# Kernel optimization log

Measured on AMD Instinct MI355X. Metric: run time of the kernel, lower is better.

Reference implementation:

```python
import jax, jax.numpy as jnp
import numpy as np

N_NODES = 50000
N_EDGES = 1_600_000
DIMS = [512, 256, 128]


def _edge_softmax(vals, rows, n):
    # sparse softmax over dim=1 (per source row), only over stored edges
    m = jax.ops.segment_max(vals, rows, num_segments=n)
    e = jnp.exp(vals - m[rows])
    s = jax.ops.segment_sum(e, rows, num_segments=n)
    return e / s[rows]


def _spmm(att, rows, cols, H, n):
    # (sparse C) @ H : gather source cols, scale by edge weight, scatter-add to rows
    return jax.ops.segment_sum(att[:, None] * H[cols], rows, num_segments=n)


def setup_inputs() -> dict:
    key = jax.random.key(0)
    ks = jax.random.split(key, 12)
    X = jax.random.normal(ks[0], (N_NODES, DIMS[0]), dtype=jnp.float32)
    edge_row = jax.random.randint(ks[1], (N_EDGES,), 0, N_NODES, dtype=jnp.int32)
    edge_col = jax.random.randint(ks[2], (N_EDGES,), 0, N_NODES, dtype=jnp.int32)
    A_vals = jnp.ones((N_EDGES,), dtype=jnp.float32)
    def lin(k, dout, din):
        lim = 1.0 / np.sqrt(din)
        return jax.random.uniform(k, (dout, din), jnp.float32, -lim, lim)
    W0 = lin(ks[3], DIMS[1], DIMS[0])
    b0 = jax.random.uniform(ks[4], (DIMS[1],), jnp.float32, -1/np.sqrt(DIMS[0]), 1/np.sqrt(DIMS[0]))
    W1 = lin(ks[5], DIMS[2], DIMS[1])
    b1 = jax.random.uniform(ks[6], (DIMS[2],), jnp.float32, -1/np.sqrt(DIMS[1]), 1/np.sqrt(DIMS[1]))
    v00 = jax.random.normal(ks[7], (DIMS[1],), dtype=jnp.float32)
    v01 = jax.random.normal(ks[8], (DIMS[1],), dtype=jnp.float32)
    v10 = jax.random.normal(ks[9], (DIMS[2],), dtype=jnp.float32)
    v11 = jax.random.normal(ks[10], (DIMS[2],), dtype=jnp.float32)
    return {"X": X, "edge_row": edge_row, "edge_col": edge_col, "A_vals": A_vals,
            "W0": W0, "b0": b0, "W1": W1, "b1": b1,
            "v00": v00, "v01": v01, "v10": v10, "v11": v11}


def reference(X, edge_row, edge_col, A_vals, W0, b0, W1, b1, v00, v01, v10, v11):
    n = X.shape[0]
    layers = [((W0, b0), (v00, v01)), ((W1, b1), (v10, v11))]
    H = X
    atts = []
    # encoder
    for (W, b), (va, vb) in layers:
        M = H @ W.T + b                               # [N, d_out]
        # attention logits are computed under no_grad in the original
        f1 = M @ va                                   # [N]
        f2 = M @ vb
        logits = jax.lax.stop_gradient(A_vals * (f1[edge_row] + f2[edge_col]))
        att = _edge_softmax(jax.nn.sigmoid(logits), edge_row, n)
        H = _spmm(att, edge_row, edge_col, M, n)
        atts.append(att)
    final_H = H
    # decoder (tied weights, reverse order, reuse encoder attention)
    for ((W, _), _), att in zip(reversed(layers), reversed(atts)):
        H = H @ W                                     # F.linear(H, W.t()) == H @ W
        H = _spmm(att, edge_row, edge_col, H, n)
    return H, final_H
```

## Files before the change

### kernel.cpp

```cpp
#include <hip/hip_runtime.h>
#include <cstdint>
#include <cstddef>

typedef __attribute__((ext_vector_type(8))) short bf16x8;
typedef __attribute__((ext_vector_type(4))) float f32x4;

__device__ __forceinline__ ushort f2b(float f) {
    union { float f; uint32_t u; } v; v.f = f;
    uint32_t r = (v.u + 0x7fffu + ((v.u >> 16) & 1u)) >> 16;
    return (ushort)r;
}
__device__ __forceinline__ float b2f(ushort b) {
    union { uint32_t u; float f; } v; v.u = ((uint32_t)b) << 16;
    return v.f;
}

__device__ __forceinline__ void gll16(const void* g, void* l) {
    __builtin_amdgcn_global_load_lds((const __attribute__((address_space(1))) void*)g,
                                     (__attribute__((address_space(3))) void*)l, 16, 0, 0);
}

__global__ __launch_bounds__(256) void hist_kernel(const int* __restrict__ rows,
                                                   int* __restrict__ bhist, int E, int nb) {
    __shared__ int h[512];
    for (int i = threadIdx.x; i < nb; i += 256) h[i] = 0;
    __syncthreads();
    int stride = gridDim.x * blockDim.x;
    for (int e = blockIdx.x * blockDim.x + threadIdx.x; e < E; e += stride)
        atomicAdd(&h[rows[e] >> 7], 1);
    __syncthreads();
    for (int i = threadIdx.x; i < nb; i += 256)
        if (h[i]) atomicAdd(&bhist[i], h[i]);
}

__global__ __launch_bounds__(512) void scan512(const int* __restrict__ bhist,
                                               int* __restrict__ boff, int* __restrict__ gcur,
                                               int* __restrict__ rp, int nb, int E, int N) {
    __shared__ int sm[512];
    int v = ((int)threadIdx.x < nb) ? bhist[threadIdx.x] : 0;
    sm[threadIdx.x] = v;
    __syncthreads();
    for (int off = 1; off < 512; off <<= 1) {
        int t = ((int)threadIdx.x >= off) ? sm[threadIdx.x - off] : 0;
        __syncthreads();
        sm[threadIdx.x] += t;
        __syncthreads();
    }
    if ((int)threadIdx.x < nb) {
        int e0 = sm[threadIdx.x] - v;
        boff[threadIdx.x] = e0;
        gcur[threadIdx.x] = e0;
    }
    if (threadIdx.x == 0) { boff[nb] = E; rp[N] = E; }
}

__global__ __launch_bounds__(256) void binpass(const int* __restrict__ rows,
                                               const int* __restrict__ cols,
                                               const float* __restrict__ avals,
                                               int* __restrict__ gcur,
                                               uint2* __restrict__ tmp, int E, int nb) {
    __shared__ int hist[512];
    __shared__ int base[512];
    int e0 = blockIdx.x * 4096;
    int nE = min(4096, E - e0);
    for (int i = threadIdx.x; i < nb; i += 256) hist[i] = 0;
    __syncthreads();
    for (int i = threadIdx.x; i < nE; i += 256)
        atomicAdd(&hist[rows[e0 + i] >> 7], 1);
    __syncthreads();
    for (int i = threadIdx.x; i < nb; i += 256) {
        int c = hist[i];
        if (c) base[i] = atomicAdd(&gcur[i], c);
        hist[i] = 0;
    }
    __syncthreads();
    for (int i = threadIdx.x; i < nE; i += 256) {
        int r = rows[e0 + i];
        int b = r >> 7;
        int loc = atomicAdd(&hist[b], 1);
        uint2 t;
        t.x = ((uint32_t)r << 16) | (uint32_t)cols[e0 + i];
        t.y = __float_as_uint(avals[e0 + i]);
        tmp[base[b] + loc] = t;
    }
}

__global__ __launch_bounds__(256) void bucketpass(const uint2* __restrict__ tmp,
                                                  const int* __restrict__ boff,
                                                  int* __restrict__ rp,
                                                  int* __restrict__ col_s,
                                                  float* __restrict__ a_s, int N) {
    __shared__ int cnt[128];
    __shared__ int pre[128];
    int b = blockIdx.x;
    int r0 = b << 7;
    int nr = min(128, N - r0);
    int t0 = boff[b], t1 = boff[b + 1];
    if ((int)threadIdx.x < 128) cnt[threadIdx.x] = 0;
    __syncthreads();
    for (int i = t0 + (int)threadIdx.x; i < t1; i += 256)
        atomicAdd(&cnt[(tmp[i].x >> 16) - r0], 1);
    __syncthreads();
    if ((int)threadIdx.x < 128) pre[threadIdx.x] = cnt[threadIdx.x];
    __syncthreads();
    for (int off = 1; off < 128; off <<= 1) {
        int t = ((int)threadIdx.x >= off && (int)threadIdx.x < 128) ? pre[threadIdx.x - off] : 0;
        __syncthreads();
        if ((int)threadIdx.x < 128) pre[threadIdx.x] += t;
        __syncthreads();
    }
    if ((int)threadIdx.x < nr) {
        int ex = pre[threadIdx.x] - cnt[threadIdx.x];
        rp[r0 + threadIdx.x] = t0 + ex;
        cnt[threadIdx.x] = t0 + ex;
    }
    __syncthreads();
    for (int i = t0 + (int)threadIdx.x; i < t1; i += 256) {
        uint2 t = tmp[i];
        int lr = (int)(t.x >> 16) - r0;
        int pos = atomicAdd(&cnt[lr], 1);
        col_s[pos] = (int)(t.x & 0xffffu);
        a_s[pos] = __uint_as_float(t.y);
    }
}

__global__ void f2b4_kernel(const float* __restrict__ src, ushort* __restrict__ dst, int n4) {
    int i = blockIdx.x * blockDim.x + threadIdx.x;
    if (i < n4) {
        float4 v = ((const float4*)src)[i];
        ushort4 o;
        o.x = f2b(v.x); o.y = f2b(v.y); o.z = f2b(v.z); o.w = f2b(v.w);
        ((ushort4*)dst)[i] = o;
    }
}

__global__ __launch_bounds__(256) void prep_weights(const float* __restrict__ W0,
                                                    const float* __restrict__ W1,
                                                    ushort* __restrict__ W0h,
                                                    ushort* __restrict__ W1h,
                                                    ushort* __restrict__ Wt0h) {
    int i = blockIdx.x * 256 + threadIdx.x;
    float4 v = ((const float4*)W0)[i];
    ushort4 o;
    o.x = f2b(v.x); o.y = f2b(v.y); o.z = f2b(v.z); o.w = f2b(v.w);
    ((ushort4*)W0h)[i] = o;
    int r = (i * 4) >> 9;
    int c = (i * 4) & 511;
    Wt0h[(size_t)(c + 0) * 256 + r] = o.x;
    Wt0h[(size_t)(c + 1) * 256 + r] = o.y;
    Wt0h[(size_t)(c + 2) * 256 + r] = o.z;
    Wt0h[(size_t)(c + 3) * 256 + r] = o.w;
    if (i < 8192) {
        float4 w = ((const float4*)W1)[i];
        ushort4 p;
        p.x = f2b(w.x); p.y = f2b(w.y); p.z = f2b(w.z); p.w = f2b(w.w);
        ((ushort4*)W1h)[i] = p;
    }
}

__global__ __launch_bounds__(256) void gemm_bf16(const ushort* __restrict__ A,
                                                 const ushort* __restrict__ B,
                                                 const float* __restrict__ bias,
                                                 float* __restrict__ Cf,
                                                 ushort* __restrict__ Ch,
                                                 int M, int K, int Dout) {
    __shared__ ushort As[128 * 64];
    __shared__ ushort Bs[128 * 64];
    int bm = blockIdx.y * 128, bn = blockIdx.x * 128;
    int tid = threadIdx.x;
    int w = tid >> 6, l = tid & 63;
    int wm = (w & 1) * 64, wn = (w >> 1) * 64;
    int lm = l & 15, quad = l >> 4;
    int wslot = tid & 192;

    f32x4 acc[4][4] = {};

    for (int k0 = 0; k0 < K; k0 += 64) {
#pragma unroll
        for (int it = 0; it < 4; ++it) {
            int slot = it * 256 + tid;
            int row = slot >> 3;
            int qg = ((slot & 7) ^ (row & 7)) * 8;
            int ga = bm + row; if (ga > M - 1) ga = M - 1;
            gll16(A + (size_t)ga * K + k0 + qg, As + (size_t)(it * 256 + wslot) * 8);
            gll16(B + (size_t)(bn + row) * K + k0 + qg, Bs + (size_t)(it * 256 + wslot) * 8);
        }
        __syncthreads();
#pragma unroll
        for (int ks = 0; ks < 2; ++ks) {
            bf16x8 af[4], bfr[4];
#pragma unroll
            for (int i = 0; i < 4; ++i) {
                int r = wm + i * 16 + lm;
                af[i] = *(const bf16x8*)&As[r * 64 + (((ks * 4 + quad) ^ (r & 7)) * 8)];
            }
#pragma unroll
            for (int j = 0; j < 4; ++j) {
                int r = wn + j * 16 + lm;
                bfr[j] = *(const bf16x8*)&Bs[r * 64 + (((ks * 4 + quad) ^ (r & 7)) * 8)];
            }
#pragma unroll
            for (int i = 0; i < 4; ++i)
#pragma unroll
                for (int j = 0; j < 4; ++j)
                    acc[i][j] = __builtin_amdgcn_mfma_f32_16x16x32_bf16(af[i], bfr[j], acc[i][j], 0, 0, 0);
        }
        __syncthreads();
    }

    float bv[4] = {0.f, 0.f, 0.f, 0.f};
    if (bias) {
#pragma unroll
        for (int j = 0; j < 4; ++j) bv[j] = bias[bn + wn + j * 16 + lm];
    }
#pragma unroll
    for (int i = 0; i < 4; ++i) {
#pragma unroll
        for (int r = 0; r < 4; ++r) {
            int row = bm + wm + i * 16 + quad * 4 + r;
            if (row < M) {
#pragma unroll
                for (int j = 0; j < 4; ++j) {
                    int col = bn + wn + j * 16 + lm;
                    float v = acc[i][j][r] + bv[j];
                    if (Cf) Cf[(size_t)row * Dout + col] = v;
                    if (Ch) Ch[(size_t)row * Dout + col] = f2b(v);
                }
            }
        }
    }
}

__global__ __launch_bounds__(256) void fvec256_kernel(const ushort* __restrict__ Mh,
                                                      const float* __restrict__ va,
                                                      const float* __restrict__ vb,
                                                      float* __restrict__ f1,
                                                      float* __restrict__ f2, int N) {
    int n = blockIdx.x * 4 + (threadIdx.x >> 6);
    if (n >= N) return;
    int lane = threadIdx.x & 63;
    ushort4 m4 = ((const ushort4*)(Mh + (size_t)n * 256))[lane];
    float4 a4 = ((const float4*)va)[lane];
    float4 b4 = ((const float4*)vb)[lane];
    float m0 = b2f(m4.x), m1 = b2f(m4.y), m2 = b2f(m4.z), m3 = b2f(m4.w);
    float s1 = m0 * a4.x + m1 * a4.y + m2 * a4.z + m3 * a4.w;
    float s2 = m0 * b4.x + m1 * b4.y + m2 * b4.z + m3 * b4.w;
#pragma unroll
    for (int off = 32; off > 0; off >>= 1) {
        s1 += __shfl_xor(s1, off);
        s2 += __shfl_xor(s2, off);
    }
    if (lane == 0) { f1[n] = s1; f2[n] = s2; }
}

__global__ __launch_bounds__(256) void att2_kernel(const int* __restrict__ rp,
                                                   const int* __restrict__ col_s,
                                                   const float* __restrict__ a_s,
                                                   const float* __restrict__ f1,
                                                   const float* __restrict__ f2,
                                                   float* __restrict__ att,
                                                   float* __restrict__ rs, int N) {
    int r = blockIdx.x * 4 + (threadIdx.x >> 6);
    if (r >= N) return;
    int lane = threadIdx.x & 63;
    int beg = rp[r], end = rp[r + 1];
    float fr = f1[r];
    float s = 0.f;
    for (int j = beg + lane; j < end; j += 64) {
        float x = a_s[j] * (fr + f2[col_s[j]]);
        float v = 1.f / (1.f + __expf(-x));
        float e = __expf(v);
        att[j] = e;
        s += e;
    }
#pragma unroll
    for (int off = 32; off > 0; off >>= 1) s += __shfl_xor(s, off);
    if (lane == 0) rs[r] = (end > beg) ? 1.f / s : 0.f;
}

__global__ __launch_bounds__(256) void spmm128(const int* __restrict__ rp,
                                               const int* __restrict__ col_s,
                                               const float* __restrict__ att,
                                               const float* __restrict__ rs,
                                               const ushort* __restrict__ H,
                                               const float* __restrict__ bias,
                                               const float* __restrict__ va,
                                               const float* __restrict__ vb,
                                               float* __restrict__ f1,
                                               float* __restrict__ f2,
                                               ushort* __restrict__ Oh,
                                               float* __restrict__ Of, int N) {
    int r = blockIdx.x * 16 + (threadIdx.x >> 4);
    if (r >= N) return;
    int lane = threadIdx.x & 15;
    int beg = rp[r], end = rp[r + 1];
    float acc[8] = {0.f, 0.f, 0.f, 0.f, 0.f, 0.f, 0.f, 0.f};
    const uint4* H4 = (const uint4*)H;
#define FMA8(h, wgt) { \
        acc[0] += (wgt) * b2f((ushort)((h).x & 0xffffu)); \
        acc[1] += (wgt) * b2f((ushort)((h).x >> 16)); \
        acc[2] += (wgt) * b2f((ushort)((h).y & 0xffffu)); \
        acc[3] += (wgt) * b2f((ushort)((h).y >> 16)); \
        acc[4] += (wgt) * b2f((ushort)((h).z & 0xffffu)); \
        acc[5] += (wgt) * b2f((ushort)((h).z >> 16)); \
        acc[6] += (wgt) * b2f((ushort)((h).w & 0xffffu)); \
        acc[7] += (wgt) * b2f((ushort)((h).w >> 16)); }
    int j = beg;
    for (; j + 4 <= end; j += 4) {
        int c0 = col_s[j], c1 = col_s[j + 1], c2 = col_s[j + 2], c3 = col_s[j + 3];
        float w0 = att[j], w1 = att[j + 1], w2 = att[j + 2], w3 = att[j + 3];
        uint4 h0 = H4[(size_t)c0 * 16 + lane];
        uint4 h1 = H4[(size_t)c1 * 16 + lane];
        uint4 h2 = H4[(size_t)c2 * 16 + lane];
        uint4 h3 = H4[(size_t)c3 * 16 + lane];
        FMA8(h0, w0) FMA8(h1, w1) FMA8(h2, w2) FMA8(h3, w3)
    }
    for (; j < end; ++j) {
        uint4 h = H4[(size_t)col_s[j] * 16 + lane];
        float w0 = att[j];
        FMA8(h, w0)
    }
#undef FMA8
    float rsv = rs[r];
#pragma unroll
    for (int k = 0; k < 8; ++k) acc[k] *= rsv;
    if (bias) {
        const float4* b4 = (const float4*)(bias + lane * 8);
        float4 ba = b4[0], bb = b4[1];
        acc[0] += ba.x; acc[1] += ba.y; acc[2] += ba.z; acc[3] += ba.w;
        acc[4] += bb.x; acc[5] += bb.y; acc[6] += bb.z; acc[7] += bb.w;
    }
    if (va) {
        const float4* a4 = (const float4*)(va + lane * 8);
        const float4* c4 = (const float4*)(vb + lane * 8);
        float4 va0 = a4[0], va1 = a4[1], vb0 = c4[0], vb1 = c4[1];
        float p1 = acc[0] * va0.x + acc[1] * va0.y + acc[2] * va0.z + acc[3] * va0.w
                 + acc[4] * va1.x + acc[5] * va1.y + acc[6] * va1.z + acc[7] * va1.w;
        float p2 = acc[0] * vb0.x + acc[1] * vb0.y + acc[2] * vb0.z + acc[3] * vb0.w
                 + acc[4] * vb1.x + acc[5] * vb1.y + acc[6] * vb1.z + acc[7] * vb1.w;
#pragma unroll
        for (int off = 8; off > 0; off >>= 1) {
            p1 += __shfl_xor(p1, off);
            p2 += __shfl_xor(p2, off);
        }
        if (lane == 0) { f1[r] = p1; f2[r] = p2; }
    }
    if (Oh) {
        uint4 o;
        o.x = (uint32_t)f2b(acc[0]) | ((uint32_t)f2b(acc[1]) << 16);
        o.y = (uint32_t)f2b(acc[2]) | ((uint32_t)f2b(acc[3]) << 16);
        o.z = (uint32_t)f2b(acc[4]) | ((uint32_t)f2b(acc[5]) << 16);
        o.w = (uint32_t)f2b(acc[6]) | ((uint32_t)f2b(acc[7]) << 16);
        ((uint4*)Oh)[(size_t)r * 16 + lane] = o;
    }
    if (Of) {
        float4* O4 = (float4*)Of;
        O4[(size_t)r * 32 + lane * 2]     = make_float4(acc[0], acc[1], acc[2], acc[3]);
        O4[(size_t)r * 32 + lane * 2 + 1] = make_float4(acc[4], acc[5], acc[6], acc[7]);
    }
}

extern "C" void kernel_launch(void* const* d_in, const int* in_sizes, int n_in,
                              void* d_out, int out_size, void* d_ws, size_t ws_size,
                              hipStream_t stream) {
    const float* X    = (const float*)d_in[0];
    const int*   erow = (const int*)d_in[1];
    const int*   ecol = (const int*)d_in[2];
    const float* aval = (const float*)d_in[3];
    const float* W0   = (const float*)d_in[4];
    const float* b0   = (const float*)d_in[5];
    const float* W1   = (const float*)d_in[6];
    const float* b1   = (const float*)d_in[7];
    const float* v00  = (const float*)d_in[8];
    const float* v01  = (const float*)d_in[9];
    const float* v10  = (const float*)d_in[10];
    const float* v11  = (const float*)d_in[11];

    const int D0 = 512, D1 = 256, D2 = 128;
    const int N = in_sizes[0] / D0;
    const int E = in_sizes[1];
    const int NB = (N + 127) / 128;
    float* out = (float*)d_out;

    char* ws = (char*)d_ws;
    size_t off = 0;
    auto alloc = [&](size_t bytes) {
        char* p = ws + off;
        off += (bytes + 255) & ~(size_t)255;
        return p;
    };
    ushort* Xh   = (ushort*)alloc((size_t)N * D0 * 2);
    ushort* M0h  = (ushort*)alloc((size_t)N * D1 * 2);
    ushort* Ph   = (ushort*)alloc((size_t)N * D2 * 2);
    ushort* M1h  = (ushort*)alloc((size_t)N * D2 * 2);
    ushort* H2h  = (ushort*)alloc((size_t)N * D2 * 2);
    ushort* S0h  = (ushort*)alloc((size_t)N * D2 * 2);
    ushort* W0h  = (ushort*)alloc((size_t)D1 * D0 * 2);
    ushort* W1h  = (ushort*)alloc((size_t)D2 * D1 * 2);
    ushort* Wt0h = (ushort*)alloc((size_t)D0 * D1 * 2);
    ushort* WfTh = (ushort*)alloc((size_t)D0 * D2 * 2);
    float* att0  = (float*)alloc((size_t)E * 4);
    float* att1  = (float*)alloc((size_t)E * 4);
    float* a_s   = (float*)alloc((size_t)E * 4);
    float* f1    = (float*)alloc((size_t)N * 4);
    float* f2    = (float*)alloc((size_t)N * 4);
    float* rs0   = (float*)alloc((size_t)N * 4);
    float* rs1   = (float*)alloc((size_t)N * 4);
    int* rp      = (int*)alloc(((size_t)N + 1) * 4);
    int* col_s   = (int*)alloc((size_t)E * 4);
    uint2* tmp   = (uint2*)alloc((size_t)E * 8);
    int* bhist   = (int*)alloc(512 * 4);
    int* boff    = (int*)alloc(513 * 4);
    int* gcur    = (int*)alloc(512 * 4);

    hipMemsetAsync(bhist, 0, 512 * sizeof(int), stream);
    hist_kernel<<<256, 256, 0, stream>>>(erow, bhist, E, NB);
    scan512<<<1, 512, 0, stream>>>(bhist, boff, gcur, rp, NB, E, N);
    binpass<<<(E + 4095) / 4096, 256, 0, stream>>>(erow, ecol, aval, gcur, tmp, E, NB);
    bucketpass<<<NB, 256, 0, stream>>>(tmp, boff, rp, col_s, a_s, N);

    f2b4_kernel<<<((N * D0 / 4) + 255) / 256, 256, 0, stream>>>(X, Xh, N * D0 / 4);
    prep_weights<<<128, 256, 0, stream>>>(W0, W1, W0h, W1h, Wt0h);

    gemm_bf16<<<dim3(1, 4), 256, 0, stream>>>(Wt0h, W1h, nullptr, nullptr, WfTh, D0, D1, D2);

    const int gy = (N + 127) / 128;
    const int agrid = (N + 3) / 4;
    const int sgrid = (N + 15) / 16;

    gemm_bf16<<<dim3(D1 / 128, gy), 256, 0, stream>>>(Xh, W0h, b0, nullptr, M0h, N, D0, D1);
    fvec256_kernel<<<agrid, 256, 0, stream>>>(M0h, v00, v01, f1, f2, N);
    att2_kernel<<<agrid, 256, 0, stream>>>(rp, col_s, a_s, f1, f2, att0, rs0, N);
    gemm_bf16<<<dim3(1, gy), 256, 0, stream>>>(M0h, W1h, nullptr, nullptr, Ph, N, D1, D2);
    spmm128<<<sgrid, 256, 0, stream>>>(rp, col_s, att0, rs0, Ph, b1, v10, v11, f1, f2,
                                       M1h, nullptr, N);
    att2_kernel<<<agrid, 256, 0, stream>>>(rp, col_s, a_s, f1, f2, att1, rs1, N);
    spmm128<<<sgrid, 256, 0, stream>>>(rp, col_s, att1, rs1, M1h, nullptr,
                                       nullptr, nullptr, nullptr, nullptr,
                                       H2h, out + (size_t)N * D0, N);

    spmm128<<<sgrid, 256, 0, stream>>>(rp, col_s, att1, rs1, H2h, nullptr,
                                       nullptr, nullptr, nullptr, nullptr,
                                       Ph, nullptr, N);
    spmm128<<<sgrid, 256, 0, stream>>>(rp, col_s, att0, rs0, Ph, nullptr,
                                       nullptr, nullptr, nullptr, nullptr,
                                       S0h, nullptr, N);
    gemm_bf16<<<dim3(D0 / 128, gy), 256, 0, stream>>>(S0h, WfTh, nullptr, out, nullptr, N, D2, D0);
}
```

Measured before the change: 655.8 us.

## Fold first-layer linear maps into precomputed weights and fuse X conversion with logits

The change uses linearity to skip materialising M0 = X W0^T + b0. The attention logit vectors become X·(W0^T v) + b0·v, computed inside the X-to-bf16 conversion pass. The second-layer projection uses a precomputed fused weight W1·W0 with bias W1·b0, so one GEMM over K=512 replaces two GEMMs (512→256 and 256→128) plus a separate reduction kernel. This removes the M0 write and readback and a kernel launch. In exchange the reduction now runs on fp32 X, and bf16 rounding of the fused weight product changes numerics slightly.

```diff
diff --git a/kernel.cpp b/kernel.cpp
--- a/kernel.cpp
+++ b/kernel.cpp
@@ -124,26 +124,92 @@
     }
 }
 
-__global__ void f2b4_kernel(const float* __restrict__ src, ushort* __restrict__ dst, int n4) {
-    int i = blockIdx.x * blockDim.x + threadIdx.x;
-    if (i < n4) {
-        float4 v = ((const float4*)src)[i];
-        ushort4 o;
-        o.x = f2b(v.x); o.y = f2b(v.y); o.z = f2b(v.z); o.w = f2b(v.w);
-        ((ushort4*)dst)[i] = o;
+__global__ __launch_bounds__(256) void wprep(const float* __restrict__ W0,
+                                             const float* __restrict__ W1,
+                                             const float* __restrict__ b0,
+                                             const float* __restrict__ v00,
+                                             const float* __restrict__ v01,
+                                             float* __restrict__ u0,
+                                             float* __restrict__ u1,
+                                             float* __restrict__ bp,
+                                             float* __restrict__ cc) {
+    if (blockIdx.x == 0) {
+        int c = threadIdx.x;
+        for (int rep = 0; rep < 2; ++rep, c += 256) {
+            float s0 = 0.f, s1 = 0.f;
+            for (int r = 0; r < 256; ++r) {
+                float w = W0[(size_t)r * 512 + c];
+                s0 += w * v00[r];
+                s1 += w * v01[r];
+            }
+            u0[c] = s0;
+            u1[c] = s1;
+        }
+    } else {
+        int i = threadIdx.x;
+        if (i < 128) {
+            float s = 0.f;
+            for (int k = 0; k < 256; ++k) s += W1[(size_t)i * 256 + k] * b0[k];
+            bp[i] = s;
+        } else if (i == 128) {
+            float s = 0.f;
+            for (int k = 0; k < 256; ++k) s += b0[k] * v00[k];
+            cc[0] = s;
+        } else if (i == 129) {
+            float s = 0.f;
+            for (int k = 0; k < 256; ++k) s += b0[k] * v01[k];
+            cc[1] = s;
+        }
+    }
+}
+
+__global__ __launch_bounds__(256) void convert_fx(const float* __restrict__ X,
+                                                  const float* __restrict__ u0,
+                                                  const float* __restrict__ u1,
+                                                  const float* __restrict__ cc,
+                                                  ushort* __restrict__ Xh,
+                                                  float* __restrict__ f1,
+                                                  float* __restrict__ f2, int N) {
+    int w = threadIdx.x >> 6;
+    int l = threadIdx.x & 63;
+    const float4* U0 = (const float4*)u0;
+    const float4* U1 = (const float4*)u1;
+    float4 ua = U0[l * 2], ub = U0[l * 2 + 1];
+    float4 va = U1[l * 2], vb = U1[l * 2 + 1];
+    float c0 = cc[0], c1 = cc[1];
+#pragma unroll
+    for (int rr = 0; rr < 2; ++rr) {
+        int row = blockIdx.x * 8 + w * 2 + rr;
+        if (row >= N) return;
+        const float4* Xr = (const float4*)(X + (size_t)row * 512);
+        float4 x0 = Xr[l * 2], x1 = Xr[l * 2 + 1];
+        ushort4 h0, h1;
+        h0.x = f2b(x0.x); h0.y = f2b(x0.y); h0.z = f2b(x0.z); h0.w = f2b(x0.w);
+        h1.x = f2b(x1.x); h1.y = f2b(x1.y); h1.z = f2b(x1.z); h1.w = f2b(x1.w);
+        ushort4* Xo = (ushort4*)(Xh + (size_t)row * 512);
+        Xo[l * 2] = h0;
+        Xo[l * 2 + 1] = h1;
+        float s1 = x0.x * ua.x + x0.y * ua.y + x0.z * ua.z + x0.w * ua.w
+                 + x1.x * ub.x + x1.y * ub.y + x1.z * ub.z + x1.w * ub.w;
+        float s2 = x0.x * va.x + x0.y * va.y + x0.z * va.z + x0.w * va.w
+                 + x1.x * vb.x + x1.y * vb.y + x1.z * vb.z + x1.w * vb.w;
+#pragma unroll
+        for (int off = 32; off > 0; off >>= 1) {
+            s1 += __shfl_xor(s1, off);
+            s2 += __shfl_xor(s2, off);
+        }
+        if (l == 0) { f1[row] = s1 + c0; f2[row] = s2 + c1; }
     }
 }
 
 __global__ __launch_bounds__(256) void prep_weights(const float* __restrict__ W0,
                                                     const float* __restrict__ W1,
-                                                    ushort* __restrict__ W0h,
                                                     ushort* __restrict__ W1h,
                                                     ushort* __restrict__ Wt0h) {
     int i = blockIdx.x * 256 + threadIdx.x;
     float4 v = ((const float4*)W0)[i];
     ushort4 o;
     o.x = f2b(v.x); o.y = f2b(v.y); o.z = f2b(v.z); o.w = f2b(v.w);
-    ((ushort4*)W0h)[i] = o;
     int r = (i * 4) >> 9;
     int c = (i * 4) & 511;
     Wt0h[(size_t)(c + 0) * 256 + r] = o.x;
@@ -163,6 +229,7 @@
                                                  const float* __restrict__ bias,
                                                  float* __restrict__ Cf,
                                                  ushort* __restrict__ Ch,
+                                                 ushort* __restrict__ ChT,
                                                  int M, int K, int Dout) {
     __shared__ ushort As[128 * 64];
     __shared__ ushort Bs[128 * 64];
@@ -225,32 +292,11 @@
                     float v = acc[i][j][r] + bv[j];
                     if (Cf) Cf[(size_t)row * Dout + col] = v;
                     if (Ch) Ch[(size_t)row * Dout + col] = f2b(v);
+                    if (ChT) ChT[(size_t)col * M + row] = f2b(v);
                 }
             }
         }
     }
-}
-
-__global__ __launch_bounds__(256) void fvec256_kernel(const ushort* __restrict__ Mh,
-                                                      const float* __restrict__ va,
-                                                      const float* __restrict__ vb,
-                                                      float* __restrict__ f1,
-                                                      float* __restrict__ f2, int N) {
-    int n = blockIdx.x * 4 + (threadIdx.x >> 6);
-    if (n >= N) return;
-    int lane = threadIdx.x & 63;
-    ushort4 m4 = ((const ushort4*)(Mh + (size_t)n * 256))[lane];
-    float4 a4 = ((const float4*)va)[lane];
-    float4 b4 = ((const float4*)vb)[lane];
-    float m0 = b2f(m4.x), m1 = b2f(m4.y), m2 = b2f(m4.z), m3 = b2f(m4.w);
-    float s1 = m0 * a4.x + m1 * a4.y + m2 * a4.z + m3 * a4.w;
-    float s2 = m0 * b4.x + m1 * b4.y + m2 * b4.z + m3 * b4.w;
-#pragma unroll
-    for (int off = 32; off > 0; off >>= 1) {
-        s1 += __shfl_xor(s1, off);
-        s2 += __shfl_xor(s2, off);
-    }
-    if (lane == 0) { f1[n] = s1; f2[n] = s2; }
 }
 
 __global__ __launch_bounds__(256) void att2_kernel(const int* __restrict__ rp,
@@ -390,14 +436,13 @@
         return p;
     };
     ushort* Xh   = (ushort*)alloc((size_t)N * D0 * 2);
-    ushort* M0h  = (ushort*)alloc((size_t)N * D1 * 2);
     ushort* Ph   = (ushort*)alloc((size_t)N * D2 * 2);
     ushort* M1h  = (ushort*)alloc((size_t)N * D2 * 2);
     ushort* H2h  = (ushort*)alloc((size_t)N * D2 * 2);
     ushort* S0h  = (ushort*)alloc((size_t)N * D2 * 2);
-    ushort* W0h  = (ushort*)alloc((size_t)D1 * D0 * 2);
     ushort* W1h  = (ushort*)alloc((size_t)D2 * D1 * 2);
     ushort* Wt0h = (ushort*)alloc((size_t)D0 * D1 * 2);
+    ushort* Wph  = (ushort*)alloc((size_t)D2 * D0 * 2);
     ushort* WfTh = (ushort*)alloc((size_t)D0 * D2 * 2);
     float* att0  = (float*)alloc((size_t)E * 4);
     float* att1  = (float*)alloc((size_t)E * 4);
@@ -406,6 +451,10 @@
     float* f2    = (float*)alloc((size_t)N * 4);
     float* rs0   = (float*)alloc((size_t)N * 4);
     float* rs1   = (float*)alloc((size_t)N * 4);
+    float* u0    = (float*)alloc(512 * 4);
+    float* u1    = (float*)alloc(512 * 4);
+    float* bp    = (float*)alloc(128 * 4);
+    float* cc    = (float*)alloc(2 * 4);
     int* rp      = (int*)alloc(((size_t)N + 1) * 4);
     int* col_s   = (int*)alloc((size_t)E * 4);
     uint2* tmp   = (uint2*)alloc((size_t)E * 8);
@@ -419,19 +468,21 @@
     binpass<<<(E + 4095) / 4096, 256, 0, stream>>>(erow, ecol, aval, gcur, tmp, E, NB);
     bucketpass<<<NB, 256, 0, stream>>>(tmp, boff, rp, col_s, a_s, N);
 
-    f2b4_kernel<<<((N * D0 / 4) + 255) / 256, 256, 0, stream>>>(X, Xh, N * D0 / 4);
-    prep_weights<<<128, 256, 0, stream>>>(W0, W1, W0h, W1h, Wt0h);
-
-    gemm_bf16<<<dim3(1, 4), 256, 0, stream>>>(Wt0h, W1h, nullptr, nullptr, WfTh, D0, D1, D2);
+    wprep<<<2, 256, 0, stream>>>(W0, W1, b0, v00, v01, u0, u1, bp, cc);
+    prep_weights<<<128, 256, 0, stream>>>(W0, W1, W1h, Wt0h);
+
+    convert_fx<<<(N + 7) / 8, 256, 0, stream>>>(X, u0, u1, cc, Xh, f1, f2, N);
+
+    gemm_bf16<<<dim3(4, 1), 256, 0, stream>>>(W1h, Wt0h, nullptr, nullptr, Wph, WfTh,
+                                              D2, D1, D0);
 
     const int gy = (N + 127) / 128;
     const int agrid = (N + 3) / 4;
     const int sgrid = (N + 15) / 16;
 
-    gemm_bf16<<<dim3(D1 / 128, gy), 256, 0, stream>>>(Xh, W0h, b0, nullptr, M0h, N, D0, D1);
-    fvec256_kernel<<<agrid, 256, 0, stream>>>(M0h, v00, v01, f1, f2, N);
     att2_kernel<<<agrid, 256, 0, stream>>>(rp, col_s, a_s, f1, f2, att0, rs0, N);
-    gemm_bf16<<<dim3(1, gy), 256, 0, stream>>>(M0h, W1h, nullptr, nullptr, Ph, N, D1, D2);
+    gemm_bf16<<<dim3(1, gy), 256, 0, stream>>>(Xh, Wph, bp, nullptr, Ph, nullptr,
+                                               N, D0, D2);
     spmm128<<<sgrid, 256, 0, stream>>>(rp, col_s, att0, rs0, Ph, b1, v10, v11, f1, f2,
                                        M1h, nullptr, N);
     att2_kernel<<<agrid, 256, 0, stream>>>(rp, col_s, a_s, f1, f2, att1, rs1, N);
@@ -445,5 +496,6 @@
     spmm128<<<sgrid, 256, 0, stream>>>(rp, col_s, att0, rs0, Ph, nullptr,
                                        nullptr, nullptr, nullptr, nullptr,
                                        S0h, nullptr, N);
-    gemm_bf16<<<dim3(D0 / 128, gy), 256, 0, stream>>>(S0h, WfTh, nullptr, out, nullptr, N, D2, D0);
-}
+    gemm_bf16<<<dim3(D0 / 128, gy), 256, 0, stream>>>(S0h, WfTh, nullptr, out, nullptr,
+                                                      nullptr, N, D2, D0);
+}
```

New measurement: 661.4 us. No clear change (+0.8%).
